# Kernel tuning notes

Hardware: AMD Instinct MI355X
Metric: run time of the kernel (lower is better)

## Reference

```python
import jax, jax.numpy as jnp
import numpy as np

N, IN_FEATS, HIDDEN, N_CLASSES = 12000, 256, 256, 40
EPS = 1e-12  # F.normalize default eps


def setup_inputs() -> dict:
    key = jax.random.key(0)
    ks = jax.random.split(key, 6)
    # dense adjacency, scaled like a row-normalized graph operator
    adj = jax.random.uniform(ks[0], (N, N), jnp.float32) * (1.0 / 64.0)
    x = jax.random.normal(ks[1], (N, IN_FEATS), jnp.float32)
    # xavier-uniform-like weights, zero biases (matches init_params)
    def xavier(k, fan_in, fan_out):
        lim = np.sqrt(6.0 / (fan_in + fan_out)).astype(np.float32)
        return jax.random.uniform(k, (fan_in, fan_out), jnp.float32, -lim, lim)
    W0 = xavier(ks[2], IN_FEATS, HIDDEN)
    W1 = xavier(ks[3], HIDDEN, HIDDEN)
    W2 = xavier(ks[4], HIDDEN, N_CLASSES)
    b0 = jnp.zeros((HIDDEN,), jnp.float32)
    b1 = jnp.zeros((HIDDEN,), jnp.float32)
    b2 = jnp.zeros((N_CLASSES,), jnp.float32)
    return {"adj": adj, "x": x, "W0": W0, "b0": b0, "W1": W1, "b1": b1, "W2": W2, "b2": b2}


def _l2_normalize(h):
    # F.normalize(h): rows divided by max(||row||_2, eps)
    norm = jnp.sqrt(jnp.sum(h * h, axis=1, keepdims=True))
    return h / jnp.maximum(norm, EPS)


def reference(adj, x, W0, b0, W1, b1, W2, b2):
    # layer 0: aggregate -> linear -> bias -> relu -> l2-normalize (dropout=eval identity)
    h = _l2_normalize(jax.nn.relu((adj @ x) @ W0 + b0))
    # layer 1 (hidden)
    h = _l2_normalize(jax.nn.relu((adj @ h) @ W1 + b1))
    # output layer: no activation / normalize / dropout
    h = (adj @ h) @ W2 + b2
    return h
```

## Files before the change

kernel.cpp:

```cpp
#include <hip/hip_runtime.h>
#include <hip/hip_bf16.h>

#define M_ROWS 12000
#define K_PAD  12032
#define FEAT   256
#define NCLS   40
#define NSLICE 5
#define NTILES 188
#define NBM    47
#define PSLABE (M_ROWS * FEAT)
#define TILE_SHORTS 16384
#define HALF_SHORTS 8192

typedef __attribute__((ext_vector_type(4))) float f32x4;
typedef __attribute__((ext_vector_type(8))) short s16x8;
typedef __attribute__((ext_vector_type(4))) short s16x4;
typedef unsigned int u32;

__device__ __forceinline__ short f2bf(float f){
  __hip_bfloat16 h = __float2bfloat16(f);
  union { __hip_bfloat16 h; short s; } u; u.h = h; return u.s;
}
__device__ __forceinline__ float bf2f(short s){
  union { float f; u32 u; } v; v.u = ((u32)(unsigned short)s) << 16; return v.f;
}

__device__ __forceinline__ f32x4 mfma16(s16x8 a, s16x8 b, f32x4 c){
  return __builtin_amdgcn_mfma_f32_16x16x32_bf16(a, b, c, 0, 0, 0);
}

__device__ __forceinline__ void gl16(const void* g, void* l){
  __builtin_amdgcn_global_load_lds(
      (const __attribute__((address_space(1))) u32*)g,
      (__attribute__((address_space(3))) u32*)l, 16, 0, 0);
}

#define VM6   do { asm volatile("s_waitcnt vmcnt(6)" ::: "memory"); \
                   __builtin_amdgcn_sched_barrier(0); } while(0)
#define VM4   do { asm volatile("s_waitcnt vmcnt(4)" ::: "memory"); \
                   __builtin_amdgcn_sched_barrier(0); } while(0)
#define VM0   do { asm volatile("s_waitcnt vmcnt(0)" ::: "memory"); \
                   __builtin_amdgcn_sched_barrier(0); } while(0)
#define LGK0  do { asm volatile("s_waitcnt lgkmcnt(0)" ::: "memory"); \
                   __builtin_amdgcn_sched_barrier(0); } while(0)
#define BARR  do { __builtin_amdgcn_s_barrier(); \
                   __builtin_amdgcn_sched_barrier(0); } while(0)

__device__ __forceinline__ int swz(int r){ return (r & 3) ^ ((r >> 2) & 3); }

__global__ __launch_bounds__(256) void k_transpose_pack(const float* __restrict__ src,
                                                        short* __restrict__ Bpack){
  const int t = threadIdx.x;
  if (blockIdx.x == 375){
    short* d = Bpack + (size_t)187 * TILE_SHORTS + HALF_SHORTS + t * 32;
    s16x8 z = (s16x8)0;
    #pragma unroll
    for (int i = 0; i < 4; ++i) *(s16x8*)(d + 8*i) = z;
    return;
  }
  __shared__ float tile[32][257];
  const int r0 = blockIdx.x * 32;
  {
    const int r = t >> 3, cs = (t & 7) * 32;
    const float* s = src + (size_t)(r0 + r) * FEAT + cs;
    #pragma unroll
    for (int i = 0; i < 8; ++i){
      f32x4 v = *(const f32x4*)(s + 4*i);
      tile[r][cs + 4*i + 0] = v[0];
      tile[r][cs + 4*i + 1] = v[1];
      tile[r][cs + 4*i + 2] = v[2];
      tile[r][cs + 4*i + 3] = v[3];
    }
  }
  __syncthreads();
  const int c = t;
  const int kt = r0 >> 6, hh = (r0 >> 5) & 1, sc = swz(c);
  short* d = Bpack + (size_t)kt * TILE_SHORTS + hh * HALF_SHORTS + c * 32;
  #pragma unroll
  for (int i = 0; i < 4; ++i){
    s16x8 o;
    #pragma unroll
    for (int j = 0; j < 8; ++j) o[j] = f2bf(tile[8*i + j][c]);
    *(s16x8*)(d + ((i ^ sc) * 8)) = o;
  }
}

__global__ __launch_bounds__(512, 2) void k_gemm_l0(const float* __restrict__ adj,
                                                    const short* __restrict__ Bpack,
                                                    short* __restrict__ Apack,
                                                    short* __restrict__ Pbase){
  __shared__ __align__(16) short lds[2][4][8192];

  const int t = threadIdx.x;
  const int w = t >> 6, l = t & 63;
  const int wm = w >> 2, wn = w & 3;
  const int lr = l & 15, lg = l >> 4;

  int id = blockIdx.x;
  {
    const int xcd = id & 7, idx = id >> 3;
    id = (xcd < 3 ? xcd * 30 : 90 + (xcd - 3) * 29) + idx;
  }
  const int bm = id % NBM, s = id / NBM;
  const int row0 = bm * 256;
  const int u0  = (s < 3) ? s * 38 : 114 + (s - 3) * 37;
  const int nst = (s < 3) ? 38 : 37;

  const char* Bb = (const char*)Bpack;
  const size_t tp = (size_t)t * 16;
  short* Aw = Apack + (size_t)bm * NTILES * TILE_SHORTS;

  size_t abase[2];
  #pragma unroll
  for (int p = 0; p < 2; ++p){
    const int si = p * 512 + t;
    const int r  = si >> 2, sl = si & 3;
    int grow = row0 + r; if (grow > M_ROWS - 1) grow = M_ROWS - 1;
    abase[p] = (size_t)grow * M_ROWS + (size_t)((sl ^ swz(r)) * 8);
  }

  f32x4 av0[4], av1[4];

#define ISSUE_A0(kt) do{ \
    av0[0] = *(const f32x4*)(adj + abase[0] + (kt)*64);      \
    av0[1] = *(const f32x4*)(adj + abase[0] + (kt)*64 + 4);  \
    av0[2] = *(const f32x4*)(adj + abase[1] + (kt)*64);      \
    av0[3] = *(const f32x4*)(adj + abase[1] + (kt)*64 + 4); }while(0)
#define ISSUE_A1(kt) do{ \
    av1[0] = *(const f32x4*)(adj + abase[0] + (kt)*64 + 32);     \
    av1[1] = *(const f32x4*)(adj + abase[0] + (kt)*64 + 32 + 4); \
    av1[2] = *(const f32x4*)(adj + abase[1] + (kt)*64 + 32);     \
    av1[3] = *(const f32x4*)(adj + abase[1] + (kt)*64 + 32 + 4); }while(0)

#define CVT_WRITE_A(q, h, kt, AV) do{                                         \
    _Pragma("unroll")                                                         \
    for (int p = 0; p < 2; ++p){                                              \
      s16x8 o;                                                                \
      _Pragma("unroll")                                                       \
      for (int j = 0; j < 4; ++j){ o[j] = f2bf(AV[2*p][j]); o[4+j] = f2bf(AV[2*p+1][j]); } \
      const int si = p * 512 + t;                                             \
      *(s16x8*)&lds[q][h][si * 8] = o;                                        \
      *(s16x8*)(Aw + (size_t)(kt) * TILE_SHORTS + (h) * HALF_SHORTS + si * 8) = o; \
    } }while(0)

#define ST_BH(q, h, kt) do{                                                   \
    const char* s_ = Bb + (size_t)(kt) * 32768 + (h) * 16384 + tp;            \
    gl16(s_,        (char*)&lds[q][2+(h)][0] + w*1024);                       \
    gl16(s_ + 8192, (char*)&lds[q][2+(h)][0] + 8192 + w*1024); }while(0)

#define AF(q, h, mf) \
    (*(const s16x8*)&lds[q][h][ (wm*128 + (mf)*16 + lr) * 32 + \
      ((lg ^ swz(wm*128 + (mf)*16 + lr)) * 8) ])
#define BF(q, h, nf) \
    (*(const s16x8*)&lds[q][2+(h)][ (wn*64 + (nf)*16 + lr) * 32 + \
      ((lg ^ swz(wn*64 + (nf)*16 + lr)) * 8) ])

  f32x4 acc[8][4];
  #pragma unroll
  for (int m = 0; m < 8; ++m)
    #pragma unroll
    for (int n = 0; n < 4; ++n) acc[m][n] = (f32x4)(0.0f);

  ISSUE_A0(u0); ST_BH(0, 0, u0);
  ISSUE_A1(u0); ST_BH(0, 1, u0);
  VM6;  CVT_WRITE_A(0, 0, u0, av0);
  VM4;  CVT_WRITE_A(0, 1, u0, av1);
  LGK0;
  BARR;

  for (int t2 = 0; t2 < nst; ++t2){
    const int q = t2 & 1, qn = q ^ 1;
    const bool stg = (t2 + 1 < nst);
    const int ktn = u0 + t2 + 1;

    s16x8 bfr[4], af[4];

    #pragma unroll
    for (int n = 0; n < 4; ++n) bfr[n] = BF(q, 0, n);
    #pragma unroll
    for (int m = 0; m < 4; ++m) af[m] = AF(q, 0, m);
    if (stg){ ISSUE_A0(ktn); ST_BH(qn, 0, ktn); }
    BARR;
    __builtin_amdgcn_s_setprio(1);
    #pragma unroll
    for (int m = 0; m < 4; ++m)
      #pragma unroll
      for (int n = 0; n < 4; ++n)
        acc[m][n] = mfma16(af[m], bfr[n], acc[m][n]);
    __builtin_amdgcn_s_setprio(0);
    BARR;

    #pragma unroll
    for (int m = 0; m < 4; ++m) af[m] = AF(q, 0, m + 4);
    if (stg){ ISSUE_A1(ktn); ST_BH(qn, 1, ktn); }
    BARR;
    __builtin_amdgcn_s_setprio(1);
    #pragma unroll
    for (int m = 0; m < 4; ++m)
      #pragma unroll
      for (int n = 0; n < 4; ++n)
        acc[m + 4][n] = mfma16(af[m], bfr[n], acc[m + 4][n]);
    __builtin_amdgcn_s_setprio(0);
    BARR;

    if (stg) { VM6; } else { VM4; }
    #pragma unroll
    for (int n = 0; n < 4; ++n) bfr[n] = BF(q, 1, n);
    #pragma unroll
    for (int m = 0; m < 4; ++m) af[m] = AF(q, 1, m);
    if (stg){ CVT_WRITE_A(qn, 0, ktn, av0); }
    BARR;
    __builtin_amdgcn_s_setprio(1);
    #pragma unroll
    for (int m = 0; m < 4; ++m)
      #pragma unroll
      for (int n = 0; n < 4; ++n)
        acc[m][n] = mfma16(af[m], bfr[n], acc[m][n]);
    __builtin_amdgcn_s_setprio(0);
    BARR;

    #pragma unroll
    for (int m = 0; m < 4; ++m) af[m] = AF(q, 1, m + 4);
    if (stg){ VM4; CVT_WRITE_A(qn, 1, ktn, av1); }
    BARR;
    __builtin_amdgcn_s_setprio(1);
    #pragma unroll
    for (int m = 0; m < 4; ++m)
      #pragma unroll
      for (int n = 0; n < 4; ++n)
        acc[m + 4][n] = mfma16(af[m], bfr[n], acc[m + 4][n]);
    __builtin_amdgcn_s_setprio(0);
    if (stg) LGK0;
    BARR;
  }
#undef ISSUE_A0
#undef ISSUE_A1
#undef CVT_WRITE_A
#undef ST_BH
#undef AF
#undef BF

  short* P = Pbase + (size_t)s * PSLABE;
  #pragma unroll
  for (int m = 0; m < 8; ++m){
    const int row = row0 + wm*128 + m*16 + lg*4;
    #pragma unroll
    for (int n = 0; n < 4; ++n){
      const int col = wn*64 + n*16 + lr;
      short* pp = P + (size_t)row * FEAT + col;
      #pragma unroll
      for (int r = 0; r < 4; ++r)
        if (row + r < M_ROWS) pp[(size_t)r * FEAT] = f2bf(acc[m][n][r]);
    }
  }
}

__global__ __launch_bounds__(512, 2) void k_gemm8p(const short* __restrict__ Apack,
                                                   const short* __restrict__ Bpack,
                                                   short* __restrict__ Pbase){
  __shared__ __align__(16) short lds[2][4][8192];

  const int t = threadIdx.x;
  const int w = t >> 6, l = t & 63;
  const int wm = w >> 2, wn = w & 3;
  const int lr = l & 15, lg = l >> 4;

  int id = blockIdx.x;
  {
    const int xcd = id & 7, idx = id >> 3;
    id = (xcd < 3 ? xcd * 30 : 90 + (xcd - 3) * 29) + idx;
  }
  const int bm = id % NBM, s = id / NBM;
  const int row0 = bm * 256;
  const int u0  = (s < 3) ? s * 38 : 114 + (s - 3) * 37;
  const int nst = (s < 3) ? 38 : 37;

  const char* Ab = (const char*)(Apack + (size_t)bm * NTILES * TILE_SHORTS);
  const char* Bb = (const char*)Bpack;
  const size_t tp = (size_t)t * 16;

#define ST_AH(q, h, kt) do{                                                   \
    const char* s_ = Ab + (size_t)(kt) * 32768 + (h) * 16384 + tp;            \
    gl16(s_,        (char*)&lds[q][h][0] + w*1024);                           \
    gl16(s_ + 8192, (char*)&lds[q][h][0] + 8192 + w*1024); }while(0)
#define ST_BH(q, h, kt) do{                                                   \
    const char* s_ = Bb + (size_t)(kt) * 32768 + (h) * 16384 + tp;            \
    gl16(s_,        (char*)&lds[q][2+(h)][0] + w*1024);                       \
    gl16(s_ + 8192, (char*)&lds[q][2+(h)][0] + 8192 + w*1024); }while(0)

#define AF(q, h, mf) \
    (*(const s16x8*)&lds[q][h][ (wm*128 + (mf)*16 + lr) * 32 + \
      ((lg ^ swz(wm*128 + (mf)*16 + lr)) * 8) ])
#define BF(q, h, nf) \
    (*(const s16x8*)&lds[q][2+(h)][ (wn*64 + (nf)*16 + lr) * 32 + \
      ((lg ^ swz(wn*64 + (nf)*16 + lr)) * 8) ])

  f32x4 acc[8][4];
  #pragma unroll
  for (int m = 0; m < 8; ++m)
    #pragma unroll
    for (int n = 0; n < 4; ++n) acc[m][n] = (f32x4)(0.0f);

  ST_BH(0, 0, u0); ST_AH(0, 0, u0);
  ST_BH(0, 1, u0); ST_AH(0, 1, u0);
  VM4;
  BARR;

  for (int t2 = 0; t2 < nst; ++t2){
    const int q = t2 & 1, qn = q ^ 1;
    const bool stg = (t2 + 1 < nst);
    const int ktn = u0 + t2 + 1;

    s16x8 bfr[4], af[4];

    #pragma unroll
    for (int n = 0; n < 4; ++n) bfr[n] = BF(q, 0, n);
    #pragma unroll
    for (int m = 0; m < 4; ++m) af[m] = AF(q, 0, m);
    if (stg) ST_BH(qn, 0, ktn);
    BARR;
    __builtin_amdgcn_s_setprio(1);
    #pragma unroll
    for (int m = 0; m < 4; ++m)
      #pragma unroll
      for (int n = 0; n < 4; ++n)
        acc[m][n] = mfma16(af[m], bfr[n], acc[m][n]);
    __builtin_amdgcn_s_setprio(0);
    BARR;

    #pragma unroll
    for (int m = 0; m < 4; ++m) af[m] = AF(q, 0, m + 4);
    if (stg) ST_AH(qn, 0, ktn);
    BARR;
    __builtin_amdgcn_s_setprio(1);
    #pragma unroll
    for (int m = 0; m < 4; ++m)
      #pragma unroll
      for (int n = 0; n < 4; ++n)
        acc[m + 4][n] = mfma16(af[m], bfr[n], acc[m + 4][n]);
    __builtin_amdgcn_s_setprio(0);
    if (stg) { VM4; } else { VM0; }
    BARR;

    #pragma unroll
    for (int n = 0; n < 4; ++n) bfr[n] = BF(q, 1, n);
    #pragma unroll
    for (int m = 0; m < 4; ++m) af[m] = AF(q, 1, m);
    if (stg) ST_BH(qn, 1, ktn);
    BARR;
    __builtin_amdgcn_s_setprio(1);
    #pragma unroll
    for (int m = 0; m < 4; ++m)
      #pragma unroll
      for (int n = 0; n < 4; ++n)
        acc[m][n] = mfma16(af[m], bfr[n], acc[m][n]);
    __builtin_amdgcn_s_setprio(0);
    BARR;

    #pragma unroll
    for (int m = 0; m < 4; ++m) af[m] = AF(q, 1, m + 4);
    if (stg) ST_AH(qn, 1, ktn);
    BARR;
    __builtin_amdgcn_s_setprio(1);
    #pragma unroll
    for (int m = 0; m < 4; ++m)
      #pragma unroll
      for (int n = 0; n < 4; ++n)
        acc[m + 4][n] = mfma16(af[m], bfr[n], acc[m + 4][n]);
    __builtin_amdgcn_s_setprio(0);
    if (stg) { VM4; }
    BARR;
  }
#undef ST_AH
#undef ST_BH
#undef AF
#undef BF

  short* P = Pbase + (size_t)s * PSLABE;
  #pragma unroll
  for (int m = 0; m < 8; ++m){
    const int row = row0 + wm*128 + m*16 + lg*4;
    #pragma unroll
    for (int n = 0; n < 4; ++n){
      const int col = wn*64 + n*16 + lr;
      short* pp = P + (size_t)row * FEAT + col;
      #pragma unroll
      for (int r = 0; r < 4; ++r)
        if (row + r < M_ROWS) pp[(size_t)r * FEAT] = f2bf(acc[m][n][r]);
    }
  }
}

__global__ __launch_bounds__(256) void k_fused2(const short* __restrict__ Pb,
                                                const float* __restrict__ W,
                                                const float* __restrict__ b,
                                                short* __restrict__ Bpack){
  __shared__ float ylds[32][257];
  __shared__ float red[32][33];
  __shared__ float scale[32];
  const int t  = threadIdx.x;
  const int r0 = blockIdx.x * 32;
  {
    const int r = t >> 3, cs = (t & 7) * 32;
    const size_t off = (size_t)(r0 + r) * FEAT + cs;
    float aa[32];
    {
      const short* p0 = Pb + off;
      #pragma unroll
      for (int i4 = 0; i4 < 4; ++i4){
        s16x8 v = *(const s16x8*)(p0 + i4*8);
        #pragma unroll
        for (int e = 0; e < 8; ++e) aa[i4*8 + e] = bf2f(v[e]);
      }
    }
    #pragma unroll
    for (int s = 1; s < NSLICE; ++s){
      const short* ps = Pb + (size_t)s * PSLABE + off;
      #pragma unroll
      for (int i4 = 0; i4 < 4; ++i4){
        s16x8 v = *(const s16x8*)(ps + i4*8);
        #pragma unroll
        for (int e = 0; e < 8; ++e) aa[i4*8 + e] += bf2f(v[e]);
      }
    }
    #pragma unroll
    for (int k = 0; k < 32; ++k) ylds[r][cs + k] = aa[k];
  }
  __syncthreads();

  const int rg = t >> 5;
  const int cg = t & 31;
  float acc[4][8];
  {
    float bias[8];
    #pragma unroll
    for (int j = 0; j < 8; ++j) bias[j] = b[cg*8 + j];
    #pragma unroll
    for (int i = 0; i < 4; ++i)
      #pragma unroll
      for (int j = 0; j < 8; ++j) acc[i][j] = bias[j];
  }

  #pragma unroll 4
  for (int k = 0; k < FEAT; ++k){
    float yv[4];
    #pragma unroll
    for (int i = 0; i < 4; ++i) yv[i] = ylds[rg*4 + i][k];
    f32x4 w0 = *(const f32x4*)(W + (size_t)k * FEAT + cg*8);
    f32x4 w1 = *(const f32x4*)(W + (size_t)k * FEAT + cg*8 + 4);
    #pragma unroll
    for (int i = 0; i < 4; ++i){
      #pragma unroll
      for (int j = 0; j < 4; ++j){
        acc[i][j]     += yv[i] * w0[j];
        acc[i][4 + j] += yv[i] * w1[j];
      }
    }
  }

  #pragma unroll
  for (int i = 0; i < 4; ++i){
    float ss = 0.0f;
    #pragma unroll
    for (int j = 0; j < 8; ++j){
      float v = fmaxf(acc[i][j], 0.0f);
      acc[i][j] = v;
      ss += v * v;
    }
    red[rg*4 + i][cg] = ss;
  }
  __syncthreads();
  if (t < 32){
    float ssum = 0.0f;
    #pragma unroll
    for (int j = 0; j < 32; ++j) ssum += red[t][j];
    scale[t] = 1.0f / fmaxf(sqrtf(ssum), 1e-12f);
  }
  __syncthreads();

  float sc[4];
  #pragma unroll
  for (int i = 0; i < 4; ++i) sc[i] = scale[rg*4 + i];

  const int kb   = r0 + rg * 4;
  const int kt   = kb >> 6, hh = (kb >> 5) & 1, g = (kb >> 3) & 3, e0 = kb & 7;
  short* dbase = Bpack + (size_t)kt * TILE_SHORTS + hh * HALF_SHORTS;
  #pragma unroll
  for (int j = 0; j < 8; ++j){
    const int c = cg * 8 + j;
    s16x4 o;
    #pragma unroll
    for (int i = 0; i < 4; ++i) o[i] = f2bf(acc[i][j] * sc[i]);
    *(s16x4*)(dbase + c * 32 + ((g ^ swz(c)) * 8) + e0) = o;
  }
}

__global__ __launch_bounds__(256) void k_final2(const short* __restrict__ Pb,
                                                const float* __restrict__ W2,
                                                const float* __restrict__ b2,
                                                float* __restrict__ out){
  __shared__ float ylds[32][257];
  const int t  = threadIdx.x;
  const int r0 = blockIdx.x * 32;
  {
    const int r = t >> 3, cs = (t & 7) * 32;
    const size_t off = (size_t)(r0 + r) * FEAT + cs;
    float aa[32];
    {
      const short* p0 = Pb + off;
      #pragma unroll
      for (int i4 = 0; i4 < 4; ++i4){
        s16x8 v = *(const s16x8*)(p0 + i4*8);
        #pragma unroll
        for (int e = 0; e < 8; ++e) aa[i4*8 + e] = bf2f(v[e]);
      }
    }
    #pragma unroll
    for (int s = 1; s < NSLICE; ++s){
      const short* ps = Pb + (size_t)s * PSLABE + off;
      #pragma unroll
      for (int i4 = 0; i4 < 4; ++i4){
        s16x8 v = *(const s16x8*)(ps + i4*8);
        #pragma unroll
        for (int e = 0; e < 8; ++e) aa[i4*8 + e] += bf2f(v[e]);
      }
    }
    #pragma unroll
    for (int k = 0; k < 32; ++k) ylds[r][cs + k] = aa[k];
  }
  __syncthreads();

  #pragma unroll
  for (int e = t; e < 32 * NCLS; e += 256){
    const int r = e / NCLS, n = e % NCLS;
    float a = b2[n];
    #pragma unroll 8
    for (int k = 0; k < FEAT; ++k)
      a = fmaf(ylds[r][k], W2[(size_t)k * NCLS + n], a);
    out[(size_t)(r0 + r) * NCLS + n] = a;
  }
}

extern "C" void kernel_launch(void* const* d_in, const int* in_sizes, int n_in,
                              void* d_out, int out_size, void* d_ws, size_t ws_size,
                              hipStream_t stream){
  const float* adj = (const float*)d_in[0];
  const float* x   = (const float*)d_in[1];
  const float* W0  = (const float*)d_in[2];
  const float* b0  = (const float*)d_in[3];
  const float* W1  = (const float*)d_in[4];
  const float* b1  = (const float*)d_in[5];
  const float* W2  = (const float*)d_in[6];
  const float* b2  = (const float*)d_in[7];
  float* out = (float*)d_out;

  char* ws = (char*)d_ws;
  const size_t BPACK_BYTES = (size_t)NTILES * TILE_SHORTS * 2;
  const size_t APACK_BYTES = (size_t)NBM * NTILES * TILE_SHORTS * 2;

  short* Bpack = (short*)ws;
  short* Apack = (short*)(ws + BPACK_BYTES);
  short* P     = (short*)(ws + BPACK_BYTES + APACK_BYTES);

  const dim3 b256(256), b512(512);

  k_transpose_pack<<<376, b256, 0, stream>>>(x, Bpack);

  k_gemm_l0<<<NBM * NSLICE, b512, 0, stream>>>(adj, Bpack, Apack, P);
  k_fused2<<<375, b256, 0, stream>>>(P, W0, b0, Bpack);
  k_gemm8p<<<NBM * NSLICE, b512, 0, stream>>>(Apack, Bpack, P);
  k_fused2<<<375, b256, 0, stream>>>(P, W1, b1, Bpack);
  k_gemm8p<<<NBM * NSLICE, b512, 0, stream>>>(Apack, Bpack, P);
  k_final2<<<375, b256, 0, stream>>>(P, W2, b2, out);
}
```

Before: 502.6 us.

## Triple-buffer adjacency tiles in layer-1/2 GEMM to prefetch two stages ahead

Replaces the double-buffered shared-memory pipeline in the packed adjacency GEMM with a three-deep ring for the A (adjacency) tiles and keeps two buffers for B. A tiles are now loaded two k-steps ahead and B tiles one step ahead, with the vmcnt waits adjusted to match. The aim is to hide more of the global-memory latency of the large streamed adjacency operand. In exchange LDS use per block rises from 128KB to 160KB, which may prevent two blocks from fitting per CU despite the launch bound.

```diff
diff --git a/kernel.cpp b/kernel.cpp
--- a/kernel.cpp
+++ b/kernel.cpp
@@ -39,6 +39,8 @@
                    __builtin_amdgcn_sched_barrier(0); } while(0)
 #define VM4   do { asm volatile("s_waitcnt vmcnt(4)" ::: "memory"); \
                    __builtin_amdgcn_sched_barrier(0); } while(0)
+#define VM2   do { asm volatile("s_waitcnt vmcnt(2)" ::: "memory"); \
+                   __builtin_amdgcn_sched_barrier(0); } while(0)
 #define VM0   do { asm volatile("s_waitcnt vmcnt(0)" ::: "memory"); \
                    __builtin_amdgcn_sched_barrier(0); } while(0)
 #define LGK0  do { asm volatile("s_waitcnt lgkmcnt(0)" ::: "memory"); \
@@ -255,10 +257,11 @@
   }
 }
 
-__global__ __launch_bounds__(512, 2) void k_gemm8p(const short* __restrict__ Apack,
-                                                   const short* __restrict__ Bpack,
-                                                   short* __restrict__ Pbase){
-  __shared__ __align__(16) short lds[2][4][8192];
+__global__ __launch_bounds__(512, 2) void k_gemm_tri(const short* __restrict__ Apack,
+                                                     const short* __restrict__ Bpack,
+                                                     short* __restrict__ Pbase){
+  __shared__ __align__(16) short Alds[3][2][8192];
+  __shared__ __align__(16) short Blds[2][2][8192];
 
   const int t = threadIdx.x;
   const int w = t >> 6, l = t & 63;
@@ -279,20 +282,20 @@
   const char* Bb = (const char*)Bpack;
   const size_t tp = (size_t)t * 16;
 
-#define ST_AH(q, h, kt) do{                                                   \
+#define ST_A(buf, h, kt) do{                                                  \
     const char* s_ = Ab + (size_t)(kt) * 32768 + (h) * 16384 + tp;            \
-    gl16(s_,        (char*)&lds[q][h][0] + w*1024);                           \
-    gl16(s_ + 8192, (char*)&lds[q][h][0] + 8192 + w*1024); }while(0)
-#define ST_BH(q, h, kt) do{                                                   \
+    gl16(s_,        (char*)&Alds[buf][h][0] + w*1024);                        \
+    gl16(s_ + 8192, (char*)&Alds[buf][h][0] + 8192 + w*1024); }while(0)
+#define ST_B(q, h, kt) do{                                                    \
     const char* s_ = Bb + (size_t)(kt) * 32768 + (h) * 16384 + tp;            \
-    gl16(s_,        (char*)&lds[q][2+(h)][0] + w*1024);                       \
-    gl16(s_ + 8192, (char*)&lds[q][2+(h)][0] + 8192 + w*1024); }while(0)
-
-#define AF(q, h, mf) \
-    (*(const s16x8*)&lds[q][h][ (wm*128 + (mf)*16 + lr) * 32 + \
+    gl16(s_,        (char*)&Blds[q][h][0] + w*1024);                          \
+    gl16(s_ + 8192, (char*)&Blds[q][h][0] + 8192 + w*1024); }while(0)
+
+#define AF(buf, h, mf) \
+    (*(const s16x8*)&Alds[buf][h][ (wm*128 + (mf)*16 + lr) * 32 + \
       ((lg ^ swz(wm*128 + (mf)*16 + lr)) * 8) ])
 #define BF(q, h, nf) \
-    (*(const s16x8*)&lds[q][2+(h)][ (wn*64 + (nf)*16 + lr) * 32 + \
+    (*(const s16x8*)&Blds[q][h][ (wn*64 + (nf)*16 + lr) * 32 + \
       ((lg ^ swz(wn*64 + (nf)*16 + lr)) * 8) ])
 
   f32x4 acc[8][4];
@@ -301,23 +304,28 @@
     #pragma unroll
     for (int n = 0; n < 4; ++n) acc[m][n] = (f32x4)(0.0f);
 
-  ST_BH(0, 0, u0); ST_AH(0, 0, u0);
-  ST_BH(0, 1, u0); ST_AH(0, 1, u0);
-  VM4;
+  ST_A(0, 0, u0); ST_A(0, 1, u0);
+  ST_B(0, 0, u0);
+  ST_A(1, 0, u0 + 1);
+  ST_B(0, 1, u0);
+  ST_A(1, 1, u0 + 1);
+  VM6;
   BARR;
 
   for (int t2 = 0; t2 < nst; ++t2){
+    const int ab = t2 % 3;
+    int an = ab + 2; if (an >= 3) an -= 3;
     const int q = t2 & 1, qn = q ^ 1;
-    const bool stg = (t2 + 1 < nst);
-    const int ktn = u0 + t2 + 1;
+    const bool s1 = (t2 + 1 < nst), s2 = (t2 + 2 < nst);
+    const int k1 = u0 + t2 + 1, k2 = u0 + t2 + 2;
 
     s16x8 bfr[4], af[4];
 
     #pragma unroll
     for (int n = 0; n < 4; ++n) bfr[n] = BF(q, 0, n);
     #pragma unroll
-    for (int m = 0; m < 4; ++m) af[m] = AF(q, 0, m);
-    if (stg) ST_BH(qn, 0, ktn);
+    for (int m = 0; m < 4; ++m) af[m] = AF(ab, 0, m);
+    if (s1) ST_B(qn, 0, k1);
     BARR;
     __builtin_amdgcn_s_setprio(1);
     #pragma unroll
@@ -329,8 +337,8 @@
     BARR;
 
     #pragma unroll
-    for (int m = 0; m < 4; ++m) af[m] = AF(q, 0, m + 4);
-    if (stg) ST_AH(qn, 0, ktn);
+    for (int m = 0; m < 4; ++m) af[m] = AF(ab, 0, m + 4);
+    if (s2) ST_A(an, 0, k2);
     BARR;
     __builtin_amdgcn_s_setprio(1);
     #pragma unroll
@@ -339,14 +347,14 @@
       for (int n = 0; n < 4; ++n)
         acc[m + 4][n] = mfma16(af[m], bfr[n], acc[m + 4][n]);
     __builtin_amdgcn_s_setprio(0);
-    if (stg) { VM4; } else { VM0; }
+    if (s2) { VM6; } else if (s1) { VM4; } else { VM0; }
     BARR;
 
     #pragma unroll
     for (int n = 0; n < 4; ++n) bfr[n] = BF(q, 1, n);
     #pragma unroll
-    for (int m = 0; m < 4; ++m) af[m] = AF(q, 1, m);
-    if (stg) ST_BH(qn, 1, ktn);
+    for (int m = 0; m < 4; ++m) af[m] = AF(ab, 1, m);
+    if (s1) ST_B(qn, 1, k1);
     BARR;
     __builtin_amdgcn_s_setprio(1);
     #pragma unroll
@@ -358,8 +366,8 @@
     BARR;
 
     #pragma unroll
-    for (int m = 0; m < 4; ++m) af[m] = AF(q, 1, m + 4);
-    if (stg) ST_AH(qn, 1, ktn);
+    for (int m = 0; m < 4; ++m) af[m] = AF(ab, 1, m + 4);
+    if (s2) ST_A(an, 1, k2);
     BARR;
     __builtin_amdgcn_s_setprio(1);
     #pragma unroll
@@ -368,11 +376,11 @@
       for (int n = 0; n < 4; ++n)
         acc[m + 4][n] = mfma16(af[m], bfr[n], acc[m + 4][n]);
     __builtin_amdgcn_s_setprio(0);
-    if (stg) { VM4; }
-    BARR;
-  }
-#undef ST_AH
-#undef ST_BH
+    if (s2) { VM6; } else if (s1) { VM2; }
+    BARR;
+  }
+#undef ST_A
+#undef ST_B
 #undef AF
 #undef BF
 
@@ -568,8 +576,8 @@
 
   k_gemm_l0<<<NBM * NSLICE, b512, 0, stream>>>(adj, Bpack, Apack, P);
   k_fused2<<<375, b256, 0, stream>>>(P, W0, b0, Bpack);
-  k_gemm8p<<<NBM * NSLICE, b512, 0, stream>>>(Apack, Bpack, P);
+  k_gemm_tri<<<NBM * NSLICE, b512, 0, stream>>>(Apack, Bpack, P);
   k_fused2<<<375, b256, 0, stream>>>(P, W1, b1, Bpack);
-  k_gemm8p<<<NBM * NSLICE, b512, 0, stream>>>(Apack, Bpack, P);
+  k_gemm_tri<<<NBM * NSLICE, b512, 0, stream>>>(Apack, Bpack, P);
   k_final2<<<375, b256, 0, stream>>>(P, W2, b2, out);
 }
```

Measured after the change: 530.8 us. 5.6% more time.
